# Optimization experiments

Measured on AMD Instinct MI355X. Metric: run time of the kernel, lower is better.

## Reference

```python
import jax, jax.numpy as jnp
import numpy as np

N_CELLS = 50000
DEG = 32
NNZ = N_CELLS * DEG
D_IN = 64
D_OUT = 64
NEG_SLOPE = 0.2


def setup_inputs() -> dict:
    key = jax.random.key(0)
    k0, k1, k2, k3, k4 = jax.random.split(key, 5)
    x_source = jax.random.normal(k0, (N_CELLS, D_IN), jnp.float32)
    # COO indices of the sparse neighborhood matrix N: DEG entries per row
    edge_rows = jnp.repeat(jnp.arange(N_CELLS, dtype=jnp.int32), DEG)
    edge_cols = jax.random.randint(k1, (NNZ,), 0, N_CELLS, dtype=jnp.int32)
    neighborhood_values = jax.random.uniform(k2, (NNZ,), jnp.float32)
    # xavier_uniform-ish scales (exact init irrelevant for correctness baseline)
    W0 = jax.random.normal(k3, (D_IN, D_OUT), jnp.float32) * (1.414 / np.sqrt(D_IN))
    a0 = jax.random.normal(k4, (2 * D_OUT, 1), jnp.float32) * 0.1
    return {
        "x_source": x_source,
        "edge_rows": edge_rows,
        "edge_cols": edge_cols,
        "neighborhood_values": neighborhood_values,
        "W0": W0,
        "a0": a0,
    }


def reference(x_source, edge_rows, edge_cols, neighborhood_values, W0, a0):
    # message = X W_p  : [n_cells, d_out]
    message = x_source @ W0
    d = message.shape[1]
    # [X_i || X_j] a  ==  (X_i a_src) + (X_j a_dst); compute node-level dot first,
    # then gather per edge (avoids materializing [nnz, 2d] concat)
    a_src = a0[:d, 0]
    a_dst = a0[d:, 0]
    node_src = message @ a_src  # [n_cells]
    node_dst = message @ a_dst  # [n_cells]
    e = jax.nn.leaky_relu(node_src[edge_rows] + node_dst[edge_cols],
                          negative_slope=NEG_SLOPE)  # [nnz]
    # sparse_row_norm: divide each edge value by its row sum (softmax=False path)
    row_sum = jax.ops.segment_sum(e, edge_rows, num_segments=N_CELLS)
    att = e / row_sum[edge_rows]
    # Hadamard product N^1 \odot A_1, then SpMM with message
    vals = neighborhood_values * att  # [nnz]
    out = jax.ops.segment_sum(vals[:, None] * message[edge_cols], edge_rows,
                              num_segments=N_CELLS)  # [n_cells, d_out]
    # update_func='relu'
    return jax.nn.relu(out)
```

## Files before the change

kernel.cpp:

```cpp
#include <hip/hip_runtime.h>
#include <hip/hip_bf16.h>

#define N_CELLS 50000
#define DEG 32
#define DIM 64
#define NEG_SLOPE 0.2

__global__ __launch_bounds__(256)
void gat_nodes(const float* __restrict__ x,
               const float* __restrict__ W0,
               const float* __restrict__ a0,
               double* __restrict__ ns,
               double* __restrict__ nd) {
  __shared__ double2 p_s[DIM];

  const int tid = threadIdx.x;
  if (tid < DIM) {
    double ps = 0.0, pd = 0.0;
    const float4* w4 = (const float4*)(W0 + tid * DIM);
#pragma unroll
    for (int q = 0; q < DIM / 4; ++q) {
      float4 w = w4[q];
      ps = fma((double)w.x, (double)a0[4 * q + 0], ps);
      ps = fma((double)w.y, (double)a0[4 * q + 1], ps);
      ps = fma((double)w.z, (double)a0[4 * q + 2], ps);
      ps = fma((double)w.w, (double)a0[4 * q + 3], ps);
      pd = fma((double)w.x, (double)a0[DIM + 4 * q + 0], pd);
      pd = fma((double)w.y, (double)a0[DIM + 4 * q + 1], pd);
      pd = fma((double)w.z, (double)a0[DIM + 4 * q + 2], pd);
      pd = fma((double)w.w, (double)a0[DIM + 4 * q + 3], pd);
    }
    p_s[tid] = make_double2(ps, pd);
  }
  __syncthreads();

  const int r = blockIdx.x * 256 + tid;
  if (r >= N_CELLS) return;
  const float4* x4 = (const float4*)(x + (size_t)r * DIM);
  double s0 = 0.0, s1 = 0.0, d0 = 0.0, d1 = 0.0;
#pragma unroll
  for (int q = 0; q < DIM / 4; ++q) {
    float4 v = x4[q];
    double2 p0 = p_s[4 * q + 0], p1 = p_s[4 * q + 1];
    double2 p2 = p_s[4 * q + 2], p3 = p_s[4 * q + 3];
    s0 = fma((double)v.x, p0.x, s0); d0 = fma((double)v.x, p0.y, d0);
    s1 = fma((double)v.y, p1.x, s1); d1 = fma((double)v.y, p1.y, d1);
    s0 = fma((double)v.z, p2.x, s0); d0 = fma((double)v.z, p2.y, d0);
    s1 = fma((double)v.w, p3.x, s1); d1 = fma((double)v.w, p3.y, d1);
  }
  ns[r] = s0 + s1;
  nd[r] = d0 + d1;
}

__global__ __launch_bounds__(256)
void gat_edges(const float* __restrict__ x,
               const int* __restrict__ ecol,
               const float* __restrict__ nv,
               const float* __restrict__ W0,
               const double* __restrict__ ns,
               const double* __restrict__ nd,
               float* __restrict__ out) {
  __shared__ __align__(16) float w_s[4][DEG];
  __shared__ __align__(16) int c_s[4][DEG];
  __shared__ __align__(16) float h_s[4][DIM];

  const int lane = threadIdx.x & 63;
  const int wid = threadIdx.x >> 6;
  const int gwave = blockIdx.x * 4 + wid;
  const int nwaves = gridDim.x * 4;
  const int g = lane >> 4;
  const int l = lane & 15;

  float w0c[DIM];
#pragma unroll
  for (int k = 0; k < DIM; ++k) w0c[k] = W0[k * DIM + lane];

  for (int r = gwave; r < N_CELLS; r += nwaves) {
    double e = 0.0;
    int col = 0;
    float nvv = 0.0f;
    if (lane < DEG) {
      col = ecol[r * DEG + lane];
      nvv = nv[r * DEG + lane];
      double z = ns[r] + nd[col];
      e = (z >= 0.0) ? z : NEG_SLOPE * z;
    }
    double rs = e;
#pragma unroll
    for (int m = 16; m >= 1; m >>= 1) rs += __shfl_xor(rs, m, 64);
    if (lane < DEG) {
      w_s[wid][lane] = (float)((double)nvv * (e / rs));
      c_s[wid][lane] = col;
    }

    float4 a4 = make_float4(0.f, 0.f, 0.f, 0.f);
#pragma unroll
    for (int q = 0; q < DEG / 4; ++q) {
      int j = 4 * q + g;
      int c = c_s[wid][j];
      float w = w_s[wid][j];
      float4 xv = ((const float4*)x)[(size_t)c * (DIM / 4) + l];
      a4.x = fmaf(w, xv.x, a4.x);
      a4.y = fmaf(w, xv.y, a4.y);
      a4.z = fmaf(w, xv.z, a4.z);
      a4.w = fmaf(w, xv.w, a4.w);
    }
#pragma unroll
    for (int m = 16; m <= 32; m <<= 1) {
      a4.x += __shfl_xor(a4.x, m, 64);
      a4.y += __shfl_xor(a4.y, m, 64);
      a4.z += __shfl_xor(a4.z, m, 64);
      a4.w += __shfl_xor(a4.w, m, 64);
    }
    if (lane < 16) ((float4*)h_s[wid])[l] = a4;

    float o = 0.0f;
    const float4* h4p = (const float4*)h_s[wid];
#pragma unroll
    for (int q = 0; q < DIM / 4; ++q) {
      float4 h4 = h4p[q];
      o = fmaf(h4.x, w0c[4 * q + 0], o);
      o = fmaf(h4.y, w0c[4 * q + 1], o);
      o = fmaf(h4.z, w0c[4 * q + 2], o);
      o = fmaf(h4.w, w0c[4 * q + 3], o);
    }
    o = fmaxf(o, 0.0f);
    out[(size_t)r * DIM + lane] = o;
  }
}

extern "C" void kernel_launch(void* const* d_in, const int* in_sizes, int n_in,
                              void* d_out, int out_size, void* d_ws, size_t ws_size,
                              hipStream_t stream) {
  const float* x = (const float*)d_in[0];
  const int* ecol = (const int*)d_in[2];
  const float* nv = (const float*)d_in[3];
  const float* W0 = (const float*)d_in[4];
  const float* a0 = (const float*)d_in[5];
  float* out = (float*)d_out;

  double* ns = (double*)d_ws;
  double* nd = ns + N_CELLS;

  hipLaunchKernelGGL(gat_nodes, dim3((N_CELLS + 255) / 256), dim3(256), 0, stream,
                     x, W0, a0, ns, nd);
  hipLaunchKernelGGL(gat_edges, dim3(2500), dim3(256), 0, stream,
                     x, ecol, nv, W0, ns, nd, out);
}
```

Before: 146.5 us.

## Gather neighbor features from an fp16 copy and process two rows per wave

The prep kernel now also writes an fp16 copy of x, and the edge kernel gathers neighbor rows from that half-size copy instead of fp32. This cuts the bytes moved by the random gather. Each wave now handles two rows at once, with 32 lanes per row, so all 64 lanes carry edge data and no cross-group shuffle reduction is needed. The trade-offs are the extra conversion pass over x, fewer gathered bytes in flight per load, and reduced precision in the aggregated features.

```diff
diff --git a/kernel.cpp b/kernel.cpp
--- a/kernel.cpp
+++ b/kernel.cpp
@@ -1,5 +1,5 @@
 #include <hip/hip_runtime.h>
-#include <hip/hip_bf16.h>
+#include <hip/hip_fp16.h>
 
 #define N_CELLS 50000
 #define DEG 32
@@ -7,11 +7,12 @@
 #define NEG_SLOPE 0.2
 
 __global__ __launch_bounds__(256)
-void gat_nodes(const float* __restrict__ x,
-               const float* __restrict__ W0,
-               const float* __restrict__ a0,
-               double* __restrict__ ns,
-               double* __restrict__ nd) {
+void gat_prep(const float* __restrict__ x,
+              const float* __restrict__ W0,
+              const float* __restrict__ a0,
+              __half* __restrict__ x2,
+              double* __restrict__ ns,
+              double* __restrict__ nd) {
   __shared__ double2 p_s[DIM];
 
   const int tid = threadIdx.x;
@@ -34,98 +35,101 @@
   }
   __syncthreads();
 
-  const int r = blockIdx.x * 256 + tid;
-  if (r >= N_CELLS) return;
-  const float4* x4 = (const float4*)(x + (size_t)r * DIM);
-  double s0 = 0.0, s1 = 0.0, d0 = 0.0, d1 = 0.0;
+  const int gtid = blockIdx.x * 256 + tid;
+  const int nthreads = gridDim.x * 256;
+
+  const float2* xf2 = (const float2*)x;
+  __half2* xh2 = (__half2*)x2;
+  for (int i = gtid; i < N_CELLS * DIM / 2; i += nthreads) {
+    float2 v = xf2[i];
+    xh2[i] = __float22half2_rn(v);
+  }
+
+  for (int r = gtid; r < N_CELLS; r += nthreads) {
+    const float4* x4 = (const float4*)(x + (size_t)r * DIM);
+    double s0 = 0.0, s1 = 0.0, d0 = 0.0, d1 = 0.0;
 #pragma unroll
-  for (int q = 0; q < DIM / 4; ++q) {
-    float4 v = x4[q];
-    double2 p0 = p_s[4 * q + 0], p1 = p_s[4 * q + 1];
-    double2 p2 = p_s[4 * q + 2], p3 = p_s[4 * q + 3];
-    s0 = fma((double)v.x, p0.x, s0); d0 = fma((double)v.x, p0.y, d0);
-    s1 = fma((double)v.y, p1.x, s1); d1 = fma((double)v.y, p1.y, d1);
-    s0 = fma((double)v.z, p2.x, s0); d0 = fma((double)v.z, p2.y, d0);
-    s1 = fma((double)v.w, p3.x, s1); d1 = fma((double)v.w, p3.y, d1);
+    for (int q = 0; q < DIM / 4; ++q) {
+      float4 v = x4[q];
+      double2 p0 = p_s[4 * q + 0], p1 = p_s[4 * q + 1];
+      double2 p2 = p_s[4 * q + 2], p3 = p_s[4 * q + 3];
+      s0 = fma((double)v.x, p0.x, s0); d0 = fma((double)v.x, p0.y, d0);
+      s1 = fma((double)v.y, p1.x, s1); d1 = fma((double)v.y, p1.y, d1);
+      s0 = fma((double)v.z, p2.x, s0); d0 = fma((double)v.z, p2.y, d0);
+      s1 = fma((double)v.w, p3.x, s1); d1 = fma((double)v.w, p3.y, d1);
+    }
+    ns[r] = s0 + s1;
+    nd[r] = d0 + d1;
   }
-  ns[r] = s0 + s1;
-  nd[r] = d0 + d1;
 }
 
 __global__ __launch_bounds__(256)
-void gat_edges(const float* __restrict__ x,
+void gat_edges(const __half* __restrict__ x2,
                const int* __restrict__ ecol,
                const float* __restrict__ nv,
                const float* __restrict__ W0,
                const double* __restrict__ ns,
                const double* __restrict__ nd,
                float* __restrict__ out) {
-  __shared__ __align__(16) float w_s[4][DEG];
-  __shared__ __align__(16) int c_s[4][DEG];
-  __shared__ __align__(16) float h_s[4][DIM];
+  __shared__ __align__(16) float w_s[4][2][DEG];
+  __shared__ __align__(16) int c_s[4][2][DEG];
+  __shared__ __align__(16) float h_s[4][2][DIM];
 
   const int lane = threadIdx.x & 63;
   const int wid = threadIdx.x >> 6;
-  const int gwave = blockIdx.x * 4 + wid;
-  const int nwaves = gridDim.x * 4;
-  const int g = lane >> 4;
-  const int l = lane & 15;
+  const int half = lane >> 5;
+  const int sub = lane & 31;
 
   float w0c[DIM];
 #pragma unroll
   for (int k = 0; k < DIM; ++k) w0c[k] = W0[k * DIM + lane];
 
-  for (int r = gwave; r < N_CELLS; r += nwaves) {
-    double e = 0.0;
-    int col = 0;
-    float nvv = 0.0f;
-    if (lane < DEG) {
-      col = ecol[r * DEG + lane];
-      nvv = nv[r * DEG + lane];
-      double z = ns[r] + nd[col];
-      e = (z >= 0.0) ? z : NEG_SLOPE * z;
-    }
+  const int gwave = blockIdx.x * 4 + wid;
+  const int nwaves = gridDim.x * 4;
+  const int npairs = N_CELLS / 2;
+
+  for (int p = gwave; p < npairs; p += nwaves) {
+    const int r0 = 2 * p;
+    const int myrow = r0 + half;
+
+    const int eidx = r0 * DEG + lane;
+    const int col = ecol[eidx];
+    const float nvv = nv[eidx];
+    double z = ns[myrow] + nd[col];
+    double e = (z >= 0.0) ? z : NEG_SLOPE * z;
     double rs = e;
 #pragma unroll
     for (int m = 16; m >= 1; m >>= 1) rs += __shfl_xor(rs, m, 64);
-    if (lane < DEG) {
-      w_s[wid][lane] = (float)((double)nvv * (e / rs));
-      c_s[wid][lane] = col;
+    w_s[wid][half][sub] = (float)((double)nvv * (e / rs));
+    c_s[wid][half][sub] = col;
+
+    const unsigned* xp = (const unsigned*)x2;
+    float ax = 0.0f, ay = 0.0f;
+#pragma unroll
+    for (int j = 0; j < DEG; ++j) {
+      int c = c_s[wid][half][j];
+      float w = w_s[wid][half][j];
+      unsigned pk = xp[(size_t)c * (DIM / 2) + sub];
+      float2 xv = __half22float2(*(const __half2*)&pk);
+      ax = fmaf(w, xv.x, ax);
+      ay = fmaf(w, xv.y, ay);
     }
+    ((float2*)h_s[wid][half])[sub] = make_float2(ax, ay);
 
-    float4 a4 = make_float4(0.f, 0.f, 0.f, 0.f);
-#pragma unroll
-    for (int q = 0; q < DEG / 4; ++q) {
-      int j = 4 * q + g;
-      int c = c_s[wid][j];
-      float w = w_s[wid][j];
-      float4 xv = ((const float4*)x)[(size_t)c * (DIM / 4) + l];
-      a4.x = fmaf(w, xv.x, a4.x);
-      a4.y = fmaf(w, xv.y, a4.y);
-      a4.z = fmaf(w, xv.z, a4.z);
-      a4.w = fmaf(w, xv.w, a4.w);
-    }
-#pragma unroll
-    for (int m = 16; m <= 32; m <<= 1) {
-      a4.x += __shfl_xor(a4.x, m, 64);
-      a4.y += __shfl_xor(a4.y, m, 64);
-      a4.z += __shfl_xor(a4.z, m, 64);
-      a4.w += __shfl_xor(a4.w, m, 64);
-    }
-    if (lane < 16) ((float4*)h_s[wid])[l] = a4;
-
-    float o = 0.0f;
-    const float4* h4p = (const float4*)h_s[wid];
+    float oA = 0.0f, oB = 0.0f;
+    const float4* hA = (const float4*)h_s[wid][0];
+    const float4* hB = (const float4*)h_s[wid][1];
 #pragma unroll
     for (int q = 0; q < DIM / 4; ++q) {
-      float4 h4 = h4p[q];
-      o = fmaf(h4.x, w0c[4 * q + 0], o);
-      o = fmaf(h4.y, w0c[4 * q + 1], o);
-      o = fmaf(h4.z, w0c[4 * q + 2], o);
-      o = fmaf(h4.w, w0c[4 * q + 3], o);
+      float4 a = hA[q];
+      float4 b = hB[q];
+      oA = fmaf(a.x, w0c[4 * q + 0], oA); oB = fmaf(b.x, w0c[4 * q + 0], oB);
+      oA = fmaf(a.y, w0c[4 * q + 1], oA); oB = fmaf(b.y, w0c[4 * q + 1], oB);
+      oA = fmaf(a.z, w0c[4 * q + 2], oA); oB = fmaf(b.z, w0c[4 * q + 2], oB);
+      oA = fmaf(a.w, w0c[4 * q + 3], oA); oB = fmaf(b.w, w0c[4 * q + 3], oB);
     }
-    o = fmaxf(o, 0.0f);
-    out[(size_t)r * DIM + lane] = o;
+    out[(size_t)r0 * DIM + lane] = fmaxf(oA, 0.0f);
+    out[(size_t)(r0 + 1) * DIM + lane] = fmaxf(oB, 0.0f);
   }
 }
 
@@ -139,11 +143,12 @@
   const float* a0 = (const float*)d_in[5];
   float* out = (float*)d_out;
 
-  double* ns = (double*)d_ws;
+  __half* x2 = (__half*)d_ws;
+  double* ns = (double*)((char*)d_ws + (size_t)N_CELLS * DIM * sizeof(__half));
   double* nd = ns + N_CELLS;
 
-  hipLaunchKernelGGL(gat_nodes, dim3((N_CELLS + 255) / 256), dim3(256), 0, stream,
-                     x, W0, a0, ns, nd);
+  hipLaunchKernelGGL(gat_prep, dim3(512), dim3(256), 0, stream,
+                     x, W0, a0, x2, ns, nd);
   hipLaunchKernelGGL(gat_edges, dim3(2500), dim3(256), 0, stream,
-                     x, ecol, nv, W0, ns, nd, out);
+                     x2, ecol, nv, W0, ns, nd, out);
 }
```

New measurement: 127.5 us. 1.15x faster.
